# Performance work log

Hardware: AMD Instinct MI355X
Metric: run time of the kernel (lower is better)

Reference implementation:

```python
import jax, jax.numpy as jnp
import numpy as np

N = 10000
E = 80000


def gat_layer(x, src, dst, W, a_src, a_dst, b):
    # x: [N, Fin], W: [Fin, Fout]
    xw = x @ W                              # [N, Fout]
    al_src = xw @ a_src                     # [N]
    al_dst = xw @ a_dst                     # [N]
    e = jax.nn.leaky_relu(al_src[src] + al_dst[dst], 0.2)  # [E+N]
    m = jax.lax.stop_gradient(jax.ops.segment_max(e, dst, num_segments=N))
    ex = jnp.exp(e - m[dst])
    denom = jax.ops.segment_sum(ex, dst, num_segments=N)
    alpha = ex / (denom[dst] + 1e-16)       # PyG softmax eps
    out = jax.ops.segment_sum(alpha[:, None] * xw[src], dst, num_segments=N)
    return out + b


def setup_inputs() -> dict:
    key = jax.random.key(0)
    ks = jax.random.split(key, 12)
    x = jax.random.normal(ks[0], (N, 256), dtype=jnp.float32)
    edge_index = jax.random.randint(ks[1], (2, E), 0, N, dtype=jnp.int64)
    def glorot(k, fi, fo):
        return jax.random.normal(k, (fi, fo), jnp.float32) * jnp.sqrt(2.0 / (fi + fo))
    W1 = glorot(ks[2], 256, 2048)
    W2 = glorot(ks[3], 2048, 2048)
    W3 = glorot(ks[4], 2048, 1024)
    a1s = jax.random.normal(ks[5], (2048,), jnp.float32) * 0.05
    a1d = jax.random.normal(ks[6], (2048,), jnp.float32) * 0.05
    a2s = jax.random.normal(ks[7], (2048,), jnp.float32) * 0.05
    a2d = jax.random.normal(ks[8], (2048,), jnp.float32) * 0.05
    a3s = jax.random.normal(ks[9], (1024,), jnp.float32) * 0.05
    a3d = jax.random.normal(ks[10], (1024,), jnp.float32) * 0.05
    b1 = jnp.zeros((2048,), jnp.float32)
    b2 = jnp.zeros((2048,), jnp.float32)
    b3 = jnp.zeros((1024,), jnp.float32)
    return {"x": x, "edge_index": edge_index, "W1": W1, "W2": W2, "W3": W3,
            "a1s": a1s, "a1d": a1d, "a2s": a2s, "a2d": a2d, "a3s": a3s, "a3d": a3d,
            "b1": b1, "b2": b2, "b3": b3}


def reference(x, edge_index, W1, W2, W3, a1s, a1d, a2s, a2d, a3s, a3d, b1, b2, b3):
    # add self loops (PyG GATConv default add_self_loops=True)
    loop = jnp.arange(N, dtype=edge_index.dtype)
    src = jnp.concatenate([edge_index[0], loop])
    dst = jnp.concatenate([edge_index[1], loop])
    h = jax.nn.relu(gat_layer(x, src, dst, W1, a1s, a1d, b1))
    h = jax.nn.relu(gat_layer(h, src, dst, W2, a2s, a2d, b2))
    h = jax.nn.relu(gat_layer(h, src, dst, W3, a3s, a3d, b3))
    # F.normalize(dim=1), eps=1e-12
    norm = jnp.linalg.norm(h, axis=1, keepdims=True)
    return h / jnp.maximum(norm, 1e-12)
```

## Files before the change

kernel.cpp:

```cpp
#include <hip/hip_runtime.h>
#include <hip/hip_bf16.h>
#include <math.h>


typedef __attribute__((ext_vector_type(8))) short short8;
typedef __attribute__((ext_vector_type(4))) float f32x4;

#define GLOAD_LDS16(g, l)                                            \
  __builtin_amdgcn_global_load_lds(                                  \
      (const __attribute__((address_space(1))) void*)(g),            \
      (__attribute__((address_space(3))) void*)(l), 16, 0, 0)

__device__ __forceinline__ float bf16_to_f32(ushort u) {
  return __uint_as_float(((unsigned int)u) << 16);
}

__device__ __forceinline__ float block_reduce_sum_bcast(float v) {
#pragma unroll
  for (int off = 32; off > 0; off >>= 1) v += __shfl_down(v, off, 64);
  __shared__ float tmp[4];
  __shared__ float res;
  int lane = threadIdx.x & 63, w = threadIdx.x >> 6;
  if (lane == 0) tmp[w] = v;
  __syncthreads();
  if (threadIdx.x == 0) res = tmp[0] + tmp[1] + tmp[2] + tmp[3];
  __syncthreads();
  float out = res;
  __syncthreads();
  return out;
}

__device__ __forceinline__ float block_reduce_max_bcast(float v) {
#pragma unroll
  for (int off = 32; off > 0; off >>= 1) v = fmaxf(v, __shfl_down(v, off, 64));
  __shared__ float tmpm[4];
  __shared__ float resm;
  int lane = threadIdx.x & 63, w = threadIdx.x >> 6;
  if (lane == 0) tmpm[w] = v;
  __syncthreads();
  if (threadIdx.x == 0) resm = fmaxf(fmaxf(tmpm[0], tmpm[1]), fmaxf(tmpm[2], tmpm[3]));
  __syncthreads();
  float out = resm;
  __syncthreads();
  return out;
}

__global__ void detect_kernel(const int* __restrict__ ei32, int* __restrict__ flag) {
  __shared__ int cnt;
  if (threadIdx.x == 0) cnt = 0;
  __syncthreads();
  int zeros = 0;
  for (int i = threadIdx.x; i < 1024; i += 256) {
    if (ei32[2 * i + 1] == 0) zeros++;
  }
  atomicAdd(&cnt, zeros);
  __syncthreads();
  if (threadIdx.x == 0) *flag = (cnt > 900) ? 1 : 0;
}

__global__ void convert_kernel(const void* __restrict__ ei, const int* __restrict__ flag,
                               int E, int* __restrict__ src, int* __restrict__ dst) {
  int i = blockIdx.x * blockDim.x + threadIdx.x;
  if (i >= E) return;
  if (*flag) {
    const long long* p = (const long long*)ei;
    src[i] = (int)p[i];
    dst[i] = (int)p[E + i];
  } else {
    const int* p = (const int*)ei;
    src[i] = p[i];
    dst[i] = p[E + i];
  }
}

__global__ __launch_bounds__(256) void convert_f32_bf16(const float* __restrict__ in,
                                                        __hip_bfloat16* __restrict__ out,
                                                        int n) {
  int i = blockIdx.x * blockDim.x + threadIdx.x;
  if (i < n) out[i] = __float2bfloat16(in[i]);
}

__global__ __launch_bounds__(256) void transpose_w(const float* __restrict__ W,
                                                   __hip_bfloat16* __restrict__ Wt,
                                                   int K, int Nout) {
  __shared__ float t[32][33];
  int tx = threadIdx.x & 31, ty = threadIdx.x >> 5;
  int n0 = blockIdx.x * 32, k0 = blockIdx.y * 32;
#pragma unroll
  for (int i = 0; i < 4; ++i) {
    int k = k0 + ty + i * 8;
    t[ty + i * 8][tx] = W[(size_t)k * Nout + n0 + tx];
  }
  __syncthreads();
#pragma unroll
  for (int i = 0; i < 4; ++i) {
    int n = n0 + ty + i * 8;
    Wt[(size_t)n * K + k0 + tx] = __float2bfloat16(t[tx][ty + i * 8]);
  }
}

template <bool BF16OUT>
__global__ __launch_bounds__(512, 2) void gemm_bn128(const ushort* __restrict__ A,
                                                     const ushort* __restrict__ Bt,
                                                     void* __restrict__ C,
                                                     int M, int K, int Nout) {
  constexpr int BUF = 16384 + 8192;
  extern __shared__ ushort lds[];
  const int tid = threadIdx.x;
  const int l = tid & 63, w = tid >> 6;
  const int wm = w >> 2, wn = w & 3;
  const int l15 = l & 15, lhi = l >> 4;

  int nwg = gridDim.x * gridDim.y;
  int lin = blockIdx.y * gridDim.x + blockIdx.x;
  if ((nwg & 7) == 0) lin = (lin & 7) * (nwg >> 3) + (lin >> 3);
  const int bx = lin % gridDim.x, by = lin / gridDim.x;
  const int row0 = by * 256, col0 = bx * 128;

  const int c8sw = (l & 3) ^ (((l >> 5) & 1) << 1);
  const int lrow = l >> 2;
  const int chsw = lhi ^ (((l15 >> 3) & 1) << 1);
  const int rd_off = l15 * 32 + chsw * 8;

  const int sA0 = wm * 8 + wn * 2;
  const int sB0 = w;
  const ushort* ga[2][2];
  const ushort* gb[2];
#pragma unroll
  for (int sc = 0; sc < 2; ++sc) {
#pragma unroll
    for (int j = 0; j < 2; ++j) {
      int ar = min(row0 + (sA0 + j) * 16 + lrow, M - 1);
      ga[sc][j] = A + (size_t)ar * K + sc * 32 + c8sw * 8;
    }
    gb[sc] = Bt + (size_t)(col0 + sB0 * 16 + lrow) * K + sc * 32 + c8sw * 8;
  }

#define STAGE_PH(nb, kn, sc)                                                         \
  do {                                                                               \
    GLOAD_LDS16(ga[sc][0] + (kn), &lds[(nb)*BUF + ((sA0 + 0) * 2 + (sc)) * 512]);    \
    GLOAD_LDS16(ga[sc][1] + (kn), &lds[(nb)*BUF + ((sA0 + 1) * 2 + (sc)) * 512]);    \
    GLOAD_LDS16(gb[sc] + (kn), &lds[(nb)*BUF + 16384 + (sB0 * 2 + (sc)) * 512]);     \
  } while (0)

  f32x4 acc[8][2] = {};

#define PHASE(cbase, kk, STAGE_STMT)                                                 \
  do {                                                                               \
    short8 af[8], bf[2];                                                             \
    _Pragma("unroll") for (int m = 0; m < 8; ++m)                                    \
        af[m] = *(const short8*)(cbase + ((wm * 8 + m) * 2 + (kk)) * 512 + rd_off);  \
    _Pragma("unroll") for (int n = 0; n < 2; ++n)                                    \
        bf[n] = *(const short8*)(cbase + 16384 + ((wn * 2 + n) * 2 + (kk)) * 512 + rd_off); \
    STAGE_STMT;                                                                      \
    asm volatile("s_waitcnt vmcnt(6)" ::: "memory");                                 \
    __builtin_amdgcn_s_barrier();                                                    \
    __builtin_amdgcn_s_setprio(1);                                                   \
    _Pragma("unroll") for (int m = 0; m < 8; ++m)                                    \
        _Pragma("unroll") for (int n = 0; n < 2; ++n)                                \
            acc[m][n] = __builtin_amdgcn_mfma_f32_16x16x32_bf16(                     \
                af[m], bf[n], acc[m][n], 0, 0, 0);                                   \
    __builtin_amdgcn_s_setprio(0);                                                   \
    __builtin_amdgcn_s_barrier();                                                    \
  } while (0)

  const int nt = K >> 6;
  STAGE_PH(0, 0, 0);
  STAGE_PH(0, 0, 1);
  STAGE_PH(1, 64, 0);
  STAGE_PH(1, 64, 1);
  asm volatile("s_waitcnt vmcnt(6)" ::: "memory");
  __builtin_amdgcn_s_barrier();

  int cur = 0;
  for (int t = 0; t < nt; ++t) {
    const ushort* cb = &lds[cur * BUF];
    int nb = cur + 2; if (nb >= 3) nb -= 3;
    const bool pf = (t + 2) < nt;
    const int kn = (t + 2) << 6;
    PHASE(cb, 0, if (pf) STAGE_PH(nb, kn, 0));
    PHASE(cb, 1, if (pf) STAGE_PH(nb, kn, 1));
    cur = cur + 1; if (cur == 3) cur = 0;
  }

#pragma unroll
  for (int mi = 0; mi < 8; ++mi) {
#pragma unroll
    for (int v = 0; v < 4; ++v) {
      int r = row0 + wm * 128 + mi * 16 + lhi * 4 + v;
      if (r < M) {
#pragma unroll
        for (int n = 0; n < 2; ++n) {
          size_t idx = (size_t)r * Nout + col0 + wn * 32 + n * 16 + l15;
          if (BF16OUT)
            ((__hip_bfloat16*)C)[idx] = __float2bfloat16(acc[mi][n][v]);
          else
            ((float*)C)[idx] = acc[mi][n][v];
        }
      }
    }
  }
#undef PHASE
#undef STAGE_PH
}

template <bool BF16IN>
__global__ __launch_bounds__(256) void compute_al(const void* __restrict__ xw,
                                                  const float* __restrict__ a_s,
                                                  const float* __restrict__ a_d,
                                                  float* __restrict__ als,
                                                  float* __restrict__ ald, int F) {
  int n = blockIdx.x;
  float s1 = 0.f, s2 = 0.f;
  if (BF16IN) {
    const ushort* row = (const ushort*)xw + (size_t)n * F;
    int base = threadIdx.x * 8;
    short8 v = *(const short8*)(row + base);
#pragma unroll
    for (int j = 0; j < 8; ++j) {
      float f = bf16_to_f32((ushort)v[j]);
      s1 += f * a_s[base + j];
      s2 += f * a_d[base + j];
    }
  } else {
    const float* row = (const float*)xw + (size_t)n * F;
    for (int f = threadIdx.x; f < F; f += 256) {
      float v = row[f];
      s1 += v * a_s[f];
      s2 += v * a_d[f];
    }
  }
  float r1 = block_reduce_sum_bcast(s1);
  float r2 = block_reduce_sum_bcast(s2);
  if (threadIdx.x == 0) {
    als[n] = r1;
    ald[n] = r2;
  }
}

__global__ void count_kernel(const int* __restrict__ dst, int* __restrict__ counts, int E) {
  int i = blockIdx.x * blockDim.x + threadIdx.x;
  if (i < E) atomicAdd(&counts[dst[i]], 1);
}

__global__ __launch_bounds__(1024) void scan_kernel(const int* __restrict__ counts,
                                                    int* __restrict__ rowptr,
                                                    int* __restrict__ cursor, int Nn) {
  __shared__ int part[1024];
  int tid = threadIdx.x;
  int chunk = (Nn + 1023) / 1024;
  int base = tid * chunk;
  int s = 0;
  for (int i = 0; i < chunk; ++i) {
    int idx = base + i;
    if (idx < Nn) s += counts[idx];
  }
  part[tid] = s;
  __syncthreads();
  for (int off = 1; off < 1024; off <<= 1) {
    int v = 0;
    if (tid >= off) v = part[tid - off];
    __syncthreads();
    if (tid >= off) part[tid] += v;
    __syncthreads();
  }
  int run = (tid == 0) ? 0 : part[tid - 1];
  for (int i = 0; i < chunk; ++i) {
    int idx = base + i;
    if (idx < Nn) {
      rowptr[idx] = run;
      cursor[idx] = run;
      run += counts[idx];
    }
  }
  if (tid == 1023) rowptr[Nn] = part[1023];
}

__global__ void fill_kernel(const int* __restrict__ src, const int* __restrict__ dst,
                            int* __restrict__ cursor, int* __restrict__ eidx, int E) {
  int i = blockIdx.x * blockDim.x + threadIdx.x;
  if (i < E) {
    int pos = atomicAdd(&cursor[dst[i]], 1);
    eidx[pos] = src[i];
  }
}

template <int FPT, bool BF16IN, bool BF16OUT>
__global__ __launch_bounds__(256) void aggregate(const void* __restrict__ xw,
                                                 const float* __restrict__ als,
                                                 const float* __restrict__ ald,
                                                 const int* __restrict__ rowptr,
                                                 const int* __restrict__ eidx,
                                                 const float* __restrict__ bias,
                                                 void* __restrict__ out, int F) {
  int n = blockIdx.x;
  int tid = threadIdx.x;
  int beg = rowptr[n], end = rowptr[n + 1];
  int deg = end - beg;
  float aldn = ald[n];

  float lm = -INFINITY;
  for (int j = tid; j < deg; j += 256) {
    int s = eidx[beg + j];
    float e = als[s] + aldn;
    e = (e > 0.f) ? e : 0.2f * e;
    lm = fmaxf(lm, e);
  }
  if (tid == 0) {
    float e = als[n] + aldn;
    e = (e > 0.f) ? e : 0.2f * e;
    lm = fmaxf(lm, e);
  }
  float m = block_reduce_max_bcast(lm);

  float ls = 0.f;
  for (int j = tid; j < deg; j += 256) {
    int s = eidx[beg + j];
    float e = als[s] + aldn;
    e = (e > 0.f) ? e : 0.2f * e;
    ls += expf(e - m);
  }
  if (tid == 0) {
    float e = als[n] + aldn;
    e = (e > 0.f) ? e : 0.2f * e;
    ls += expf(e - m);
  }
  float denom = block_reduce_sum_bcast(ls) + 1e-16f;
  float inv_denom = 1.f / denom;

  float acc[FPT];
#pragma unroll
  for (int i = 0; i < FPT; ++i) acc[i] = 0.f;

  __shared__ float alpha_sh[256];
  __shared__ int src_sh[256];
  int total = deg + 1;
  for (int c0 = 0; c0 < total; c0 += 256) {
    int j = c0 + tid;
    if (j < total) {
      int s = (j < deg) ? eidx[beg + j] : n;
      float e = als[s] + aldn;
      e = (e > 0.f) ? e : 0.2f * e;
      alpha_sh[tid] = expf(e - m) * inv_denom;
      src_sh[tid] = s;
    }
    __syncthreads();
    int cn = min(256, total - c0);
    for (int jj = 0; jj < cn; ++jj) {
      float al = alpha_sh[jj];
      if (BF16IN) {
        const ushort* row = (const ushort*)xw + (size_t)src_sh[jj] * F;
#pragma unroll
        for (int i = 0; i < FPT / 2; ++i) {
          unsigned int u = *(const unsigned int*)(row + tid * 2 + i * 512);
          acc[2 * i]     += al * __uint_as_float((u & 0xffffu) << 16);
          acc[2 * i + 1] += al * __uint_as_float(u & 0xffff0000u);
        }
      } else {
        const float* row = (const float*)xw + (size_t)src_sh[jj] * F;
#pragma unroll
        for (int i = 0; i < FPT; ++i) acc[i] += al * row[tid + i * 256];
      }
    }
    __syncthreads();
  }

#pragma unroll
  for (int i = 0; i < FPT; ++i) {
    int col = BF16IN ? (tid * 2 + (i >> 1) * 512 + (i & 1)) : (tid + i * 256);
    float v = fmaxf(acc[i] + bias[col], 0.f);
    size_t idx = (size_t)n * F + col;
    if (BF16OUT)
      ((__hip_bfloat16*)out)[idx] = __float2bfloat16(v);
    else
      ((float*)out)[idx] = v;
  }
}

__global__ __launch_bounds__(256) void normalize_kernel(const float* __restrict__ h,
                                                        float* __restrict__ out,
                                                        int F) {
  int n = blockIdx.x;
  const float* row = h + (size_t)n * F;
  float ss = 0.f;
  for (int f = threadIdx.x; f < F; f += 256) {
    float v = row[f];
    ss += v * v;
  }
  float tot = block_reduce_sum_bcast(ss);
  float inv = 1.f / fmaxf(sqrtf(tot), 1e-12f);
  for (int f = threadIdx.x; f < F; f += 256) {
    out[(size_t)n * F + f] = row[f] * inv;
  }
}

extern "C" void kernel_launch(void* const* d_in, const int* in_sizes, int n_in,
                              void* d_out, int out_size, void* d_ws, size_t ws_size,
                              hipStream_t stream) {
  const float* x   = (const float*)d_in[0];
  const void*  ei  = d_in[1];
  const float* W1  = (const float*)d_in[2];
  const float* W2  = (const float*)d_in[3];
  const float* W3  = (const float*)d_in[4];
  const float* a1s = (const float*)d_in[5];
  const float* a1d = (const float*)d_in[6];
  const float* a2s = (const float*)d_in[7];
  const float* a2d = (const float*)d_in[8];
  const float* a3s = (const float*)d_in[9];
  const float* a3d = (const float*)d_in[10];
  const float* b1  = (const float*)d_in[11];
  const float* b2  = (const float*)d_in[12];
  const float* b3  = (const float*)d_in[13];

  const int N = in_sizes[0] / 256;
  const int E = in_sizes[1] / 2;

  char* ws = (char*)d_ws;
  size_t off = 0;
  auto alloc = [&](size_t bytes) -> void* {
    void* p = ws + off;
    off += (bytes + 255) & ~(size_t)255;
    return p;
  };
  ushort* xwb = (ushort*)alloc((size_t)N * 2048 * 2);
  ushort* hbf = (ushort*)alloc((size_t)N * 2048 * 2);
  float* bufA = (float*)alloc((size_t)N * 1024 * 4);
  __hip_bfloat16* xb  = (__hip_bfloat16*)alloc((size_t)N * 256 * 2);
  __hip_bfloat16* Wt1 = (__hip_bfloat16*)alloc((size_t)2048 * 256 * 2);
  __hip_bfloat16* Wt2 = (__hip_bfloat16*)alloc((size_t)2048 * 2048 * 2);
  __hip_bfloat16* Wt3 = (__hip_bfloat16*)alloc((size_t)1024 * 2048 * 2);
  float* als   = (float*)alloc((size_t)N * 4);
  float* ald   = (float*)alloc((size_t)N * 4);
  int* counts  = (int*)alloc((size_t)N * 4);
  int* rowptr  = (int*)alloc((size_t)(N + 1) * 4);
  int* cursor  = (int*)alloc((size_t)N * 4);
  int* eidx    = (int*)alloc((size_t)E * 4);
  int* src32   = (int*)alloc((size_t)E * 4);
  int* dst32   = (int*)alloc((size_t)E * 4);
  int* flag    = (int*)alloc(256);

  static bool attr_done = false;
  if (!attr_done) {
    hipFuncSetAttribute((const void*)gemm_bn128<true>,
                        hipFuncAttributeMaxDynamicSharedMemorySize, 147456);
    hipFuncSetAttribute((const void*)gemm_bn128<false>,
                        hipFuncAttributeMaxDynamicSharedMemorySize, 147456);
    attr_done = true;
  }

  detect_kernel<<<1, 256, 0, stream>>>((const int*)ei, flag);
  convert_kernel<<<(E + 255) / 256, 256, 0, stream>>>(ei, flag, E, src32, dst32);
  hipMemsetAsync(counts, 0, (size_t)N * 4, stream);
  count_kernel<<<(E + 255) / 256, 256, 0, stream>>>(dst32, counts, E);
  scan_kernel<<<1, 1024, 0, stream>>>(counts, rowptr, cursor, N);
  fill_kernel<<<(E + 255) / 256, 256, 0, stream>>>(src32, dst32, cursor, eidx, E);

  convert_f32_bf16<<<(N * 256 + 255) / 256, 256, 0, stream>>>(x, xb, N * 256);
  transpose_w<<<dim3(2048 / 32, 256 / 32), 256, 0, stream>>>(W1, Wt1, 256, 2048);
  transpose_w<<<dim3(2048 / 32, 2048 / 32), 256, 0, stream>>>(W2, Wt2, 2048, 2048);
  transpose_w<<<dim3(1024 / 32, 2048 / 32), 256, 0, stream>>>(W3, Wt3, 2048, 1024);

  dim3 blk(256);
  dim3 gblk(512);
  int mb = (N + 255) / 256;

  gemm_bn128<true><<<dim3(2048 / 128, mb), gblk, 147456, stream>>>((const ushort*)xb, (const ushort*)Wt1, xwb, N, 256, 2048);
  compute_al<true><<<N, blk, 0, stream>>>(xwb, a1s, a1d, als, ald, 2048);
  aggregate<8, true, true><<<N, blk, 0, stream>>>(xwb, als, ald, rowptr, eidx, b1, hbf, 2048);

  gemm_bn128<true><<<dim3(2048 / 128, mb), gblk, 147456, stream>>>(hbf, (const ushort*)Wt2, xwb, N, 2048, 2048);
  compute_al<true><<<N, blk, 0, stream>>>(xwb, a2s, a2d, als, ald, 2048);
  aggregate<8, true, true><<<N, blk, 0, stream>>>(xwb, als, ald, rowptr, eidx, b2, hbf, 2048);

  gemm_bn128<false><<<dim3(1024 / 128, mb), gblk, 147456, stream>>>(hbf, (const ushort*)Wt3, bufA, N, 2048, 1024);
  compute_al<false><<<N, blk, 0, stream>>>(bufA, a3s, a3d, als, ald, 1024);
  float* hf32 = (float*)xwb;
  aggregate<4, false, false><<<N, blk, 0, stream>>>(bufA, als, ald, rowptr, eidx, b3, hf32, 1024);

  normalize_kernel<<<N, blk, 0, stream>>>(hf32, (float*)d_out, 1024);
}
```

Before: 465.3 us.

## Reassociate GAT layers to aggregate before the weight GEMM and precompute W·a

Uses linearity to rewrite each layer as (A·H)·W instead of A·(H·W). Attention logits now come from H·(W·a), with W·a precomputed by a new matvec kernel, and the bias plus ReLU move into the GEMM epilogue. Layer 1 now aggregates 256-wide inputs instead of 2048-wide, and layer 3 aggregates bf16 at 2048 width instead of fp32 at 1024. The inputs to the attention projection and to aggregation are rounded to bf16 in a different order, which may change accuracy slightly.

New measurement: 473.9 us. Within noise of the previous version (+1.9%).

```diff
diff --git a/kernel.cpp b/kernel.cpp
--- a/kernel.cpp
+++ b/kernel.cpp
@@ -99,9 +99,194 @@
   }
 }
 
+__global__ __launch_bounds__(256) void matvec_wa(const float* __restrict__ W,
+                                                 const float* __restrict__ a_s,
+                                                 const float* __restrict__ a_d,
+                                                 float* __restrict__ wa_s,
+                                                 float* __restrict__ wa_d, int F) {
+  int k = blockIdx.x;
+  const float* row = W + (size_t)k * F;
+  float s1 = 0.f, s2 = 0.f;
+  for (int f = threadIdx.x; f < F; f += 256) {
+    float w = row[f];
+    s1 += w * a_s[f];
+    s2 += w * a_d[f];
+  }
+  float r1 = block_reduce_sum_bcast(s1);
+  float r2 = block_reduce_sum_bcast(s2);
+  if (threadIdx.x == 0) {
+    wa_s[k] = r1;
+    wa_d[k] = r2;
+  }
+}
+
+template <int FPT>
+__global__ __launch_bounds__(256) void compute_al(const ushort* __restrict__ H,
+                                                  const float* __restrict__ wa_s,
+                                                  const float* __restrict__ wa_d,
+                                                  float* __restrict__ als,
+                                                  float* __restrict__ ald, int F) {
+  int n = blockIdx.x;
+  const ushort* row = H + (size_t)n * F;
+  float s1 = 0.f, s2 = 0.f;
+  if (FPT == 8) {
+    int base = threadIdx.x * 8;
+    short8 v = *(const short8*)(row + base);
+#pragma unroll
+    for (int j = 0; j < 8; ++j) {
+      float f = bf16_to_f32((ushort)v[j]);
+      s1 += f * wa_s[base + j];
+      s2 += f * wa_d[base + j];
+    }
+  } else {
+    float f = bf16_to_f32(row[threadIdx.x]);
+    s1 = f * wa_s[threadIdx.x];
+    s2 = f * wa_d[threadIdx.x];
+  }
+  float r1 = block_reduce_sum_bcast(s1);
+  float r2 = block_reduce_sum_bcast(s2);
+  if (threadIdx.x == 0) {
+    als[n] = r1;
+    ald[n] = r2;
+  }
+}
+
+__global__ void count_kernel(const int* __restrict__ dst, int* __restrict__ counts, int E) {
+  int i = blockIdx.x * blockDim.x + threadIdx.x;
+  if (i < E) atomicAdd(&counts[dst[i]], 1);
+}
+
+__global__ __launch_bounds__(1024) void scan_kernel(const int* __restrict__ counts,
+                                                    int* __restrict__ rowptr,
+                                                    int* __restrict__ cursor, int Nn) {
+  __shared__ int part[1024];
+  int tid = threadIdx.x;
+  int chunk = (Nn + 1023) / 1024;
+  int base = tid * chunk;
+  int s = 0;
+  for (int i = 0; i < chunk; ++i) {
+    int idx = base + i;
+    if (idx < Nn) s += counts[idx];
+  }
+  part[tid] = s;
+  __syncthreads();
+  for (int off = 1; off < 1024; off <<= 1) {
+    int v = 0;
+    if (tid >= off) v = part[tid - off];
+    __syncthreads();
+    if (tid >= off) part[tid] += v;
+    __syncthreads();
+  }
+  int run = (tid == 0) ? 0 : part[tid - 1];
+  for (int i = 0; i < chunk; ++i) {
+    int idx = base + i;
+    if (idx < Nn) {
+      rowptr[idx] = run;
+      cursor[idx] = run;
+      run += counts[idx];
+    }
+  }
+  if (tid == 1023) rowptr[Nn] = part[1023];
+}
+
+__global__ void fill_kernel(const int* __restrict__ src, const int* __restrict__ dst,
+                            int* __restrict__ cursor, int* __restrict__ eidx, int E) {
+  int i = blockIdx.x * blockDim.x + threadIdx.x;
+  if (i < E) {
+    int pos = atomicAdd(&cursor[dst[i]], 1);
+    eidx[pos] = src[i];
+  }
+}
+
+template <int FPT>
+__global__ __launch_bounds__(256) void aggregate(const ushort* __restrict__ H,
+                                                 const float* __restrict__ als,
+                                                 const float* __restrict__ ald,
+                                                 const int* __restrict__ rowptr,
+                                                 const int* __restrict__ eidx,
+                                                 ushort* __restrict__ out, int F) {
+  int n = blockIdx.x;
+  int tid = threadIdx.x;
+  int beg = rowptr[n], end = rowptr[n + 1];
+  int deg = end - beg;
+  float aldn = ald[n];
+
+  float lm = -INFINITY;
+  for (int j = tid; j < deg; j += 256) {
+    int s = eidx[beg + j];
+    float e = als[s] + aldn;
+    e = (e > 0.f) ? e : 0.2f * e;
+    lm = fmaxf(lm, e);
+  }
+  if (tid == 0) {
+    float e = als[n] + aldn;
+    e = (e > 0.f) ? e : 0.2f * e;
+    lm = fmaxf(lm, e);
+  }
+  float m = block_reduce_max_bcast(lm);
+
+  float ls = 0.f;
+  for (int j = tid; j < deg; j += 256) {
+    int s = eidx[beg + j];
+    float e = als[s] + aldn;
+    e = (e > 0.f) ? e : 0.2f * e;
+    ls += expf(e - m);
+  }
+  if (tid == 0) {
+    float e = als[n] + aldn;
+    e = (e > 0.f) ? e : 0.2f * e;
+    ls += expf(e - m);
+  }
+  float denom = block_reduce_sum_bcast(ls) + 1e-16f;
+  float inv_denom = 1.f / denom;
+
+  float acc[FPT];
+#pragma unroll
+  for (int i = 0; i < FPT; ++i) acc[i] = 0.f;
+
+  __shared__ float alpha_sh[256];
+  __shared__ int src_sh[256];
+  int total = deg + 1;
+  for (int c0 = 0; c0 < total; c0 += 256) {
+    int j = c0 + tid;
+    if (j < total) {
+      int s = (j < deg) ? eidx[beg + j] : n;
+      float e = als[s] + aldn;
+      e = (e > 0.f) ? e : 0.2f * e;
+      alpha_sh[tid] = expf(e - m) * inv_denom;
+      src_sh[tid] = s;
+    }
+    __syncthreads();
+    int cn = min(256, total - c0);
+    for (int jj = 0; jj < cn; ++jj) {
+      float al = alpha_sh[jj];
+      const ushort* row = H + (size_t)src_sh[jj] * F;
+      if (FPT == 1) {
+        acc[0] += al * bf16_to_f32(row[tid]);
+      } else {
+#pragma unroll
+        for (int i = 0; i < FPT / 2; ++i) {
+          unsigned int u = *(const unsigned int*)(row + tid * 2 + i * 512);
+          acc[2 * i]     += al * __uint_as_float((u & 0xffffu) << 16);
+          acc[2 * i + 1] += al * __uint_as_float(u & 0xffff0000u);
+        }
+      }
+    }
+    __syncthreads();
+  }
+
+#pragma unroll
+  for (int i = 0; i < FPT; ++i) {
+    int col = (FPT == 1) ? tid : (tid * 2 + (i >> 1) * 512 + (i & 1));
+    __hip_bfloat16 hv = __float2bfloat16(acc[i]);
+    out[(size_t)n * F + col] = *(ushort*)&hv;
+  }
+}
+
 template <bool BF16OUT>
 __global__ __launch_bounds__(512, 2) void gemm_bn128(const ushort* __restrict__ A,
                                                      const ushort* __restrict__ Bt,
+                                                     const float* __restrict__ bias,
                                                      void* __restrict__ C,
                                                      int M, int K, int Nout) {
   constexpr int BUF = 16384 + 8192;
@@ -191,190 +376,19 @@
       if (r < M) {
 #pragma unroll
         for (int n = 0; n < 2; ++n) {
-          size_t idx = (size_t)r * Nout + col0 + wn * 32 + n * 16 + l15;
+          int col = col0 + wn * 32 + n * 16 + l15;
+          float val = fmaxf(acc[mi][n][v] + bias[col], 0.f);
+          size_t idx = (size_t)r * Nout + col;
           if (BF16OUT)
-            ((__hip_bfloat16*)C)[idx] = __float2bfloat16(acc[mi][n][v]);
+            ((__hip_bfloat16*)C)[idx] = __float2bfloat16(val);
           else
-            ((float*)C)[idx] = acc[mi][n][v];
+            ((float*)C)[idx] = val;
         }
       }
     }
   }
 #undef PHASE
 #undef STAGE_PH
-}
-
-template <bool BF16IN>
-__global__ __launch_bounds__(256) void compute_al(const void* __restrict__ xw,
-                                                  const float* __restrict__ a_s,
-                                                  const float* __restrict__ a_d,
-                                                  float* __restrict__ als,
-                                                  float* __restrict__ ald, int F) {
-  int n = blockIdx.x;
-  float s1 = 0.f, s2 = 0.f;
-  if (BF16IN) {
-    const ushort* row = (const ushort*)xw + (size_t)n * F;
-    int base = threadIdx.x * 8;
-    short8 v = *(const short8*)(row + base);
-#pragma unroll
-    for (int j = 0; j < 8; ++j) {
-      float f = bf16_to_f32((ushort)v[j]);
-      s1 += f * a_s[base + j];
-      s2 += f * a_d[base + j];
-    }
-  } else {
-    const float* row = (const float*)xw + (size_t)n * F;
-    for (int f = threadIdx.x; f < F; f += 256) {
-      float v = row[f];
-      s1 += v * a_s[f];
-      s2 += v * a_d[f];
-    }
-  }
-  float r1 = block_reduce_sum_bcast(s1);
-  float r2 = block_reduce_sum_bcast(s2);
-  if (threadIdx.x == 0) {
-    als[n] = r1;
-    ald[n] = r2;
-  }
-}
-
-__global__ void count_kernel(const int* __restrict__ dst, int* __restrict__ counts, int E) {
-  int i = blockIdx.x * blockDim.x + threadIdx.x;
-  if (i < E) atomicAdd(&counts[dst[i]], 1);
-}
-
-__global__ __launch_bounds__(1024) void scan_kernel(const int* __restrict__ counts,
-                                                    int* __restrict__ rowptr,
-                                                    int* __restrict__ cursor, int Nn) {
-  __shared__ int part[1024];
-  int tid = threadIdx.x;
-  int chunk = (Nn + 1023) / 1024;
-  int base = tid * chunk;
-  int s = 0;
-  for (int i = 0; i < chunk; ++i) {
-    int idx = base + i;
-    if (idx < Nn) s += counts[idx];
-  }
-  part[tid] = s;
-  __syncthreads();
-  for (int off = 1; off < 1024; off <<= 1) {
-    int v = 0;
-    if (tid >= off) v = part[tid - off];
-    __syncthreads();
-    if (tid >= off) part[tid] += v;
-    __syncthreads();
-  }
-  int run = (tid == 0) ? 0 : part[tid - 1];
-  for (int i = 0; i < chunk; ++i) {
-    int idx = base + i;
-    if (idx < Nn) {
-      rowptr[idx] = run;
-      cursor[idx] = run;
-      run += counts[idx];
-    }
-  }
-  if (tid == 1023) rowptr[Nn] = part[1023];
-}
-
-__global__ void fill_kernel(const int* __restrict__ src, const int* __restrict__ dst,
-                            int* __restrict__ cursor, int* __restrict__ eidx, int E) {
-  int i = blockIdx.x * blockDim.x + threadIdx.x;
-  if (i < E) {
-    int pos = atomicAdd(&cursor[dst[i]], 1);
-    eidx[pos] = src[i];
-  }
-}
-
-template <int FPT, bool BF16IN, bool BF16OUT>
-__global__ __launch_bounds__(256) void aggregate(const void* __restrict__ xw,
-                                                 const float* __restrict__ als,
-                                                 const float* __restrict__ ald,
-                                                 const int* __restrict__ rowptr,
-                                                 const int* __restrict__ eidx,
-                                                 const float* __restrict__ bias,
-                                                 void* __restrict__ out, int F) {
-  int n = blockIdx.x;
-  int tid = threadIdx.x;
-  int beg = rowptr[n], end = rowptr[n + 1];
-  int deg = end - beg;
-  float aldn = ald[n];
-
-  float lm = -INFINITY;
-  for (int j = tid; j < deg; j += 256) {
-    int s = eidx[beg + j];
-    float e = als[s] + aldn;
-    e = (e > 0.f) ? e : 0.2f * e;
-    lm = fmaxf(lm, e);
-  }
-  if (tid == 0) {
-    float e = als[n] + aldn;
-    e = (e > 0.f) ? e : 0.2f * e;
-    lm = fmaxf(lm, e);
-  }
-  float m = block_reduce_max_bcast(lm);
-
-  float ls = 0.f;
-  for (int j = tid; j < deg; j += 256) {
-    int s = eidx[beg + j];
-    float e = als[s] + aldn;
-    e = (e > 0.f) ? e : 0.2f * e;
-    ls += expf(e - m);
-  }
-  if (tid == 0) {
-    float e = als[n] + aldn;
-    e = (e > 0.f) ? e : 0.2f * e;
-    ls += expf(e - m);
-  }
-  float denom = block_reduce_sum_bcast(ls) + 1e-16f;
-  float inv_denom = 1.f / denom;
-
-  float acc[FPT];
-#pragma unroll
-  for (int i = 0; i < FPT; ++i) acc[i] = 0.f;
-
-  __shared__ float alpha_sh[256];
-  __shared__ int src_sh[256];
-  int total = deg + 1;
-  for (int c0 = 0; c0 < total; c0 += 256) {
-    int j = c0 + tid;
-    if (j < total) {
-      int s = (j < deg) ? eidx[beg + j] : n;
-      float e = als[s] + aldn;
-      e = (e > 0.f) ? e : 0.2f * e;
-      alpha_sh[tid] = expf(e - m) * inv_denom;
-      src_sh[tid] = s;
-    }
-    __syncthreads();
-    int cn = min(256, total - c0);
-    for (int jj = 0; jj < cn; ++jj) {
-      float al = alpha_sh[jj];
-      if (BF16IN) {
-        const ushort* row = (const ushort*)xw + (size_t)src_sh[jj] * F;
-#pragma unroll
-        for (int i = 0; i < FPT / 2; ++i) {
-          unsigned int u = *(const unsigned int*)(row + tid * 2 + i * 512);
-          acc[2 * i]     += al * __uint_as_float((u & 0xffffu) << 16);
-          acc[2 * i + 1] += al * __uint_as_float(u & 0xffff0000u);
-        }
-      } else {
-        const float* row = (const float*)xw + (size_t)src_sh[jj] * F;
-#pragma unroll
-        for (int i = 0; i < FPT; ++i) acc[i] += al * row[tid + i * 256];
-      }
-    }
-    __syncthreads();
-  }
-
-#pragma unroll
-  for (int i = 0; i < FPT; ++i) {
-    int col = BF16IN ? (tid * 2 + (i >> 1) * 512 + (i & 1)) : (tid + i * 256);
-    float v = fmaxf(acc[i] + bias[col], 0.f);
-    size_t idx = (size_t)n * F + col;
-    if (BF16OUT)
-      ((__hip_bfloat16*)out)[idx] = __float2bfloat16(v);
-    else
-      ((float*)out)[idx] = v;
-  }
 }
 
 __global__ __launch_bounds__(256) void normalize_kernel(const float* __restrict__ h,
@@ -422,13 +436,19 @@
     off += (bytes + 255) & ~(size_t)255;
     return p;
   };
-  ushort* xwb = (ushort*)alloc((size_t)N * 2048 * 2);
-  ushort* hbf = (ushort*)alloc((size_t)N * 2048 * 2);
-  float* bufA = (float*)alloc((size_t)N * 1024 * 4);
-  __hip_bfloat16* xb  = (__hip_bfloat16*)alloc((size_t)N * 256 * 2);
+  ushort* h    = (ushort*)alloc((size_t)N * 2048 * 2);
+  ushort* hagg = (ushort*)alloc((size_t)N * 2048 * 2);
+  float* hf32  = (float*)alloc((size_t)N * 1024 * 4);
+  ushort* xb   = (ushort*)alloc((size_t)N * 256 * 2);
   __hip_bfloat16* Wt1 = (__hip_bfloat16*)alloc((size_t)2048 * 256 * 2);
   __hip_bfloat16* Wt2 = (__hip_bfloat16*)alloc((size_t)2048 * 2048 * 2);
   __hip_bfloat16* Wt3 = (__hip_bfloat16*)alloc((size_t)1024 * 2048 * 2);
+  float* wa1s = (float*)alloc(256 * 4);
+  float* wa1d = (float*)alloc(256 * 4);
+  float* wa2s = (float*)alloc(2048 * 4);
+  float* wa2d = (float*)alloc(2048 * 4);
+  float* wa3s = (float*)alloc(2048 * 4);
+  float* wa3d = (float*)alloc(2048 * 4);
   float* als   = (float*)alloc((size_t)N * 4);
   float* ald   = (float*)alloc((size_t)N * 4);
   int* counts  = (int*)alloc((size_t)N * 4);
@@ -455,27 +475,29 @@
   scan_kernel<<<1, 1024, 0, stream>>>(counts, rowptr, cursor, N);
   fill_kernel<<<(E + 255) / 256, 256, 0, stream>>>(src32, dst32, cursor, eidx, E);
 
-  convert_f32_bf16<<<(N * 256 + 255) / 256, 256, 0, stream>>>(x, xb, N * 256);
+  convert_f32_bf16<<<(N * 256 + 255) / 256, 256, 0, stream>>>(x, (__hip_bfloat16*)xb, N * 256);
   transpose_w<<<dim3(2048 / 32, 256 / 32), 256, 0, stream>>>(W1, Wt1, 256, 2048);
   transpose_w<<<dim3(2048 / 32, 2048 / 32), 256, 0, stream>>>(W2, Wt2, 2048, 2048);
   transpose_w<<<dim3(1024 / 32, 2048 / 32), 256, 0, stream>>>(W3, Wt3, 2048, 1024);
+  matvec_wa<<<256, 256, 0, stream>>>(W1, a1s, a1d, wa1s, wa1d, 2048);
+  matvec_wa<<<2048, 256, 0, stream>>>(W2, a2s, a2d, wa2s, wa2d, 2048);
+  matvec_wa<<<2048, 256, 0, stream>>>(W3, a3s, a3d, wa3s, wa3d, 1024);
 
   dim3 blk(256);
   dim3 gblk(512);
   int mb = (N + 255) / 256;
 
-  gemm_bn128<true><<<dim3(2048 / 128, mb), gblk, 147456, stream>>>((const ushort*)xb, (const ushort*)Wt1, xwb, N, 256, 2048);
-  compute_al<true><<<N, blk, 0, stream>>>(xwb, a1s, a1d, als, ald, 2048);
-  aggregate<8, true, true><<<N, blk, 0, stream>>>(xwb, als, ald, rowptr, eidx, b1, hbf, 2048);
-
-  gemm_bn128<true><<<dim3(2048 / 128, mb), gblk, 147456, stream>>>(hbf, (const ushort*)Wt2, xwb, N, 2048, 2048);
-  compute_al<true><<<N, blk, 0, stream>>>(xwb, a2s, a2d, als, ald, 2048);
-  aggregate<8, true, true><<<N, blk, 0, stream>>>(xwb, als, ald, rowptr, eidx, b2, hbf, 2048);
-
-  gemm_bn128<false><<<dim3(1024 / 128, mb), gblk, 147456, stream>>>(hbf, (const ushort*)Wt3, bufA, N, 2048, 1024);
-  compute_al<false><<<N, blk, 0, stream>>>(bufA, a3s, a3d, als, ald, 1024);
-  float* hf32 = (float*)xwb;
-  aggregate<4, false, false><<<N, blk, 0, stream>>>(bufA, als, ald, rowptr, eidx, b3, hf32, 1024);
+  compute_al<1><<<N, blk, 0, stream>>>(xb, wa1s, wa1d, als, ald, 256);
+  aggregate<1><<<N, blk, 0, stream>>>(xb, als, ald, rowptr, eidx, hagg, 256);
+  gemm_bn128<true><<<dim3(2048 / 128, mb), gblk, 147456, stream>>>(hagg, (const ushort*)Wt1, b1, h, N, 256, 2048);
+
+  compute_al<8><<<N, blk, 0, stream>>>(h, wa2s, wa2d, als, ald, 2048);
+  aggregate<8><<<N, blk, 0, stream>>>(h, als, ald, rowptr, eidx, hagg, 2048);
+  gemm_bn128<true><<<dim3(2048 / 128, mb), gblk, 147456, stream>>>(hagg, (const ushort*)Wt2, b2, h, N, 2048, 2048);
+
+  compute_al<8><<<N, blk, 0, stream>>>(h, wa3s, wa3d, als, ald, 2048);
+  aggregate<8><<<N, blk, 0, stream>>>(h, als, ald, rowptr, eidx, hagg, 2048);
+  gemm_bn128<false><<<dim3(1024 / 128, mb), gblk, 147456, stream>>>(hagg, (const ushort*)Wt3, b3, hf32, N, 2048, 1024);
 
   normalize_kernel<<<N, blk, 0, stream>>>(hf32, (float*)d_out, 1024);
 }
```
